# Kernel tuning notes

Hardware: AMD Instinct MI355X
Metric: run time of the kernel (lower is better)

The kernel has to match this reference:

```python
import jax, jax.numpy as jnp
import numpy as np
import math

WINDOW = 512
N_HEAD = 16

def setup_inputs() -> dict:
    key = jax.random.key(0)
    ks = jax.random.split(key, 5)
    B, L, D = 2, 4096, 1024
    s = 0.02
    return {
        "x": jax.random.normal(ks[0], (B, L, D), dtype=jnp.float32),
        "Wq": jax.random.normal(ks[1], (D, D), dtype=jnp.float32) * s,
        "bq": jnp.zeros((D,), jnp.float32),
        "Wk": jax.random.normal(ks[2], (D, D), dtype=jnp.float32) * s,
        "bk": jnp.zeros((D,), jnp.float32),
        "Wv": jax.random.normal(ks[3], (D, D), dtype=jnp.float32) * s,
        "bv": jnp.zeros((D,), jnp.float32),
        "Wo": jax.random.normal(ks[4], (D, D), dtype=jnp.float32) * s,
        "bo": jnp.zeros((D,), jnp.float32),
    }

def reference(x, Wq, bq, Wk, bk, Wv, bv, Wo, bo):
    # Chunked sliding-window MHA (eval mode, dropout inactive).
    B, L, D = x.shape
    W, H = WINDOW, N_HEAD
    dh = D // H
    C = L // W  # number of query chunks
    scale = 1.0 / math.sqrt(dh)

    # Project full sequence once (linear, per-token -> identical math).
    q = x @ Wq.T + bq
    k = x @ Wk.T + bk
    v = x @ Wv.T + bv

    # Pad K/V by one window at the front so every chunk sees 2W keys.
    kp = jnp.pad(k, ((0, 0), (W, 0), (0, 0)))
    vp = jnp.pad(v, ((0, 0), (W, 0), (0, 0)))
    idx = jnp.arange(C)[:, None] * W + jnp.arange(2 * W)[None, :]  # [C, 2W] into padded seq
    kc = kp[:, idx].reshape(B, C, 2 * W, H, dh)
    vc = vp[:, idx].reshape(B, C, 2 * W, H, dh)
    qc = q.reshape(B, C, W, H, dh)

    scores = jnp.einsum('bcqhd,bckhd->bchqk', qc, kc) * scale  # [B,C,H,W,2W]
    valid = (idx >= W)  # padded positions (chunk 0's lookback) are invalid
    scores = jnp.where(valid[None, :, None, None, :], scores, jnp.float32(-1e9))
    attn = jax.nn.softmax(scores, axis=-1)
    out = jnp.einsum('bchqk,bckhd->bcqhd', attn, vc).reshape(B, L, D)
    return out @ Wo.T + bo
```

## Files before the change

kernel.cpp:

```cpp
#include <hip/hip_runtime.h>
#include <hip/hip_bf16.h>

typedef __hip_bfloat16 bf16;
typedef __attribute__((ext_vector_type(8))) short bf16x8;
typedef __attribute__((ext_vector_type(4))) float f32x4;
typedef unsigned int u32;
typedef unsigned short u16;

#define MFMA(a,b,c) __builtin_amdgcn_mfma_f32_16x16x32_bf16((a),(b),(c),0,0,0)

__device__ __forceinline__ u16 f32_to_bf16_rtne(float f) {
  u32 b = __builtin_bit_cast(u32, f);
  b += 0x7FFFu + ((b >> 16) & 1u);
  return (u16)(b >> 16);
}
__device__ __forceinline__ u32 pk2bf(float a, float b) {
  u32 ua = __builtin_bit_cast(u32, a); ua += 0x7FFFu + ((ua >> 16) & 1u);
  u32 ub = __builtin_bit_cast(u32, b); ub += 0x7FFFu + ((ub >> 16) & 1u);
  return __builtin_amdgcn_perm(ub, ua, 0x07060302u);
}
__device__ __forceinline__ u32 pk2bf_rtz(float a, float b) {
  return __builtin_amdgcn_perm(__builtin_bit_cast(u32, b),
                               __builtin_bit_cast(u32, a), 0x07060302u);
}
__device__ __forceinline__ uint4 cvt8(uint4 lo, uint4 hi) {
  const float4 fl = __builtin_bit_cast(float4, lo);
  const float4 fh = __builtin_bit_cast(float4, hi);
  uint4 r;
  r.x = pk2bf(fl.x, fl.y); r.y = pk2bf(fl.z, fl.w);
  r.z = pk2bf(fh.x, fh.y); r.w = pk2bf(fh.z, fh.w);
  return r;
}

__device__ __forceinline__ void barrier_lgkm() {
  asm volatile("s_waitcnt lgkmcnt(0)\n\ts_barrier" ::: "memory");
}
__device__ __forceinline__ void barrier_plain() {
  asm volatile("s_barrier" ::: "memory");
}

typedef const __attribute__((address_space(1))) void* gas_ptr;
typedef __attribute__((address_space(3))) void* las_ptr;
__device__ __forceinline__ void gload_lds16(const void* g, void* l) {
  __builtin_amdgcn_global_load_lds((gas_ptr)g, (las_ptr)l, 16, 0, 0);
}

static constexpr float SL2E = 0.125f * 1.44269504f;

__global__ __launch_bounds__(256)
void cast_all(const float* __restrict__ wq, const float* __restrict__ wk,
              const float* __restrict__ wv, const float* __restrict__ wo,
              const float* __restrict__ x,
              u16* __restrict__ wqkv, u16* __restrict__ wob,
              u16* __restrict__ xb) {
  const size_t DD8 = (size_t)1024 * 1024 / 8;
  if (blockIdx.x < 2048) {
    const int m = blockIdx.x >> 9;
    const size_t i = ((size_t)(blockIdx.x & 511)) * 256 + threadIdx.x;
    const float* src = (m == 0) ? wq : (m == 1) ? wk : (m == 2) ? wv : wo;
    u16* dst = (m < 3) ? (wqkv + (size_t)m * DD8 * 8) : wob;
    const float4* s = (const float4*)src + i * 2;
    ((uint4*)dst)[i] = cvt8(__builtin_bit_cast(uint4, s[0]),
                            __builtin_bit_cast(uint4, s[1]));
  } else {
    const size_t i = ((size_t)(blockIdx.x - 2048)) * 256 + threadIdx.x;
    const float4* s = (const float4*)x + i * 2;
    ((uint4*)xb)[i] = cvt8(__builtin_bit_cast(uint4, s[0]),
                           __builtin_bit_cast(uint4, s[1]));
  }
}

template <int MODE>
__global__ __launch_bounds__(512, 2)
void gemm8p(const bf16* __restrict__ A, const bf16* __restrict__ W,
            const float* __restrict__ b0, const float* __restrict__ b1,
            const float* __restrict__ b2, void* __restrict__ o0,
            void* __restrict__ o1, void* __restrict__ o2,
            int M, int N, int K)
{
  __shared__ __align__(16) bf16 AsB[2][128 * 64];
  __shared__ __align__(16) bf16 BsB[2][256 * 64];

  const int nwg = gridDim.x * gridDim.y;
  const int raw = blockIdx.y * gridDim.x + blockIdx.x;
  const int vwg = (raw & 7) * (nwg >> 3) + (raw >> 3);
  const int NT  = gridDim.y;
  const int bx  = vwg / NT, by = vwg - bx * NT;
  const int m0  = bx * 128, n0 = by * 256;

  const int tid  = threadIdx.x;
  const int wv   = tid >> 6, lane = tid & 63;
  const int quad = lane >> 4, l16 = lane & 15;
  const int wm   = wv >> 2, wn = wv & 3;
  const int r7   = l16 & 7;

  const int rr = tid >> 3, g = tid & 7;
  const int sg8 = (g ^ (rr & 7)) * 8;
  const bf16* aS = A + (size_t)(m0 + rr) * K + sg8;
  const bf16* wS = W + (size_t)(n0 + rr) * K + sg8;
  const int ldstW = wv * 512;

#define STA8(buf, kt) do { \
    gload_lds16(aS + (size_t)(kt) * 64,                      &AsB[buf][ldstW]); \
    gload_lds16(aS + (size_t)64 * K + (size_t)(kt) * 64,     &AsB[buf][4096 + ldstW]); \
  } while (0)
#define STB8(buf, kt) do { \
    gload_lds16(wS + (size_t)(kt) * 64,                      &BsB[buf][ldstW]); \
    gload_lds16(wS + (size_t)64 * K + (size_t)(kt) * 64,     &BsB[buf][4096 + ldstW]); \
    gload_lds16(wS + (size_t)128 * K + (size_t)(kt) * 64,    &BsB[buf][8192 + ldstW]); \
    gload_lds16(wS + (size_t)192 * K + (size_t)(kt) * 64,    &BsB[buf][12288 + ldstW]); \
  } while (0)

  int aoff[4], boff[4];
#pragma unroll
  for (int mt = 0; mt < 4; ++mt) aoff[mt] = (wm * 64 + mt * 16 + l16) * 64;
#pragma unroll
  for (int nt = 0; nt < 4; ++nt) boff[nt] = (wn * 64 + nt * 16 + l16) * 64;
  const int k0o = (quad ^ r7) * 8;
  const int k1o = ((4 + quad) ^ r7) * 8;

  f32x4 acc[4][4] = {};
  bf16x8 bfr[4][2], afr[2][2];

  const int nk = K >> 6;

  STA8(0, 0);
  STB8(0, 0);
  STB8(1, 1);
  asm volatile("s_waitcnt vmcnt(4)\n\ts_barrier" ::: "memory");

  for (int t = 0; t < nk; ++t) {
    const int c = t & 1;
    const bf16* Ac = AsB[c];
    const bf16* Bc = BsB[c];

#pragma unroll
    for (int nt = 0; nt < 4; ++nt) {
      bfr[nt][0] = *(const bf16x8*)(Bc + boff[nt] + k0o);
      bfr[nt][1] = *(const bf16x8*)(Bc + boff[nt] + k1o);
    }
#pragma unroll
    for (int mt = 0; mt < 2; ++mt) {
      afr[mt][0] = *(const bf16x8*)(Ac + aoff[mt] + k0o);
      afr[mt][1] = *(const bf16x8*)(Ac + aoff[mt] + k1o);
    }
    if (t + 1 < nk) STA8((t + 1) & 1, t + 1);
    barrier_plain();
    __builtin_amdgcn_s_setprio(1);
#pragma unroll
    for (int mt = 0; mt < 2; ++mt)
#pragma unroll
      for (int nt = 0; nt < 4; ++nt) {
        acc[mt][nt] = MFMA(afr[mt][0], bfr[nt][0], acc[mt][nt]);
        acc[mt][nt] = MFMA(afr[mt][1], bfr[nt][1], acc[mt][nt]);
      }
    __builtin_amdgcn_s_setprio(0);
    barrier_lgkm();

#pragma unroll
    for (int mt = 0; mt < 2; ++mt) {
      afr[mt][0] = *(const bf16x8*)(Ac + aoff[mt + 2] + k0o);
      afr[mt][1] = *(const bf16x8*)(Ac + aoff[mt + 2] + k1o);
    }
    if (t + 2 < nk) STB8(c, t + 2);
    barrier_plain();
    __builtin_amdgcn_s_setprio(1);
#pragma unroll
    for (int mt = 0; mt < 2; ++mt)
#pragma unroll
      for (int nt = 0; nt < 4; ++nt) {
        acc[mt + 2][nt] = MFMA(afr[mt][0], bfr[nt][0], acc[mt + 2][nt]);
        acc[mt + 2][nt] = MFMA(afr[mt][1], bfr[nt][1], acc[mt + 2][nt]);
      }
    __builtin_amdgcn_s_setprio(0);
    if (t + 1 < nk) {
      if (t + 2 < nk)
        asm volatile("s_waitcnt vmcnt(4) lgkmcnt(0)\n\ts_barrier" ::: "memory");
      else
        asm volatile("s_waitcnt vmcnt(0) lgkmcnt(0)\n\ts_barrier" ::: "memory");
    }
  }
#undef STA8
#undef STB8

  const int band = n0 >> 10;
  const float* bias = (band == 0) ? b0 : (band == 1) ? b1 : b2;
#pragma unroll
  for (int nt = 0; nt < 4; ++nt) {
    const int col = n0 + wn * 64 + nt * 16 + l16;
    const int cl  = col & 1023;
    const float bv = bias[cl];
#pragma unroll
    for (int mt = 0; mt < 4; ++mt) {
      const int rbase = m0 + wm * 64 + mt * 16 + quad * 4;
      if (MODE == 1) {
#pragma unroll
        for (int r = 0; r < 4; ++r)
          ((float*)o0)[(size_t)(rbase + r) * N + col] = acc[mt][nt][r] + bv;
      } else if (band == 2) {
        const int hh = cl >> 6, dd = cl & 63;
        const int bb = rbase >> 12, tl = rbase & 4095;
        u16* dst = (u16*)o2 + ((size_t)((bb * 16 + hh) * 64 + dd)) * 4096 + tl;
        uint2 pk;
        pk.x = pk2bf(acc[mt][nt][0] + bv, acc[mt][nt][1] + bv);
        pk.y = pk2bf(acc[mt][nt][2] + bv, acc[mt][nt][3] + bv);
        *(uint2*)dst = pk;
      } else {
        u16* dst = (u16*)((band == 0) ? o0 : o1);
        const float sc = (band == 0) ? SL2E : 1.0f;
#pragma unroll
        for (int r = 0; r < 4; ++r)
          dst[(size_t)(rbase + r) * 1024 + cl] =
              f32_to_bf16_rtne((acc[mt][nt][r] + bv) * sc);
      }
    }
  }
}

__global__ __launch_bounds__(256)
void attn_swin(const bf16* __restrict__ qb, const bf16* __restrict__ kb,
               const bf16* __restrict__ vtb, u16* __restrict__ ctx)
{
  __shared__ __align__(16) bf16 Ks[2][64 * 72];
  __shared__ __align__(16) bf16 Vts[2][64 * 72];

  int bid = blockIdx.x;
  const int g  = bid & 255, qt = bid >> 8;
  const int h  = g & 15, c = (g >> 4) & 7, b = g >> 7;

  const int tid  = threadIdx.x;
  const int w    = tid >> 6, lane = tid & 63;
  const int quad = lane >> 4, l16 = lane & 15;

  const int tq0  = c * 512 + qt * 128;
  const int hoff = h * 64;
  const int kstart = (c == 0) ? 0 : (c - 1) * 512;
  const int nkt    = (c == 0) ? 8 : 16;

  bf16x8 qf[2][2];
#pragma unroll
  for (int u = 0; u < 2; ++u) {
    const bf16* qr = qb + ((size_t)(b * 4096 + tq0 + w * 32 + u * 16 + l16)) * 1024 + hoff;
    qf[u][0] = *(const bf16x8*)(qr + quad * 8);
    qf[u][1] = *(const bf16x8*)(qr + 32 + quad * 8);
  }

  const int m    = tid >> 2;
  const int cseg = (tid & 3) * 16;
  const int sig  = (((m >> 4) & 1) << 5) | (((m >> 2) & 3) << 3)
                 | (((m >> 5) & 1) << 2) | (m & 3);
  const bf16* kgp = kb + ((size_t)(b * 4096 + kstart + sig)) * 1024 + hoff + cseg;
  const bf16* vgp = vtb + ((size_t)((b * 16 + h) * 64 + m)) * 4096 + kstart + cseg;
  const int soff = m * 72 + cseg;

  float l_i[2] = {0.f, 0.f};
  f32x4 o[2][4] = {};

  uint4 ka0 = *(const uint4*)(kgp), ka1 = *(const uint4*)(kgp + 8);
  uint4 va0 = *(const uint4*)(vgp), va1 = *(const uint4*)(vgp + 8);
  kgp += (size_t)64 * 1024; vgp += 64;
  *(uint4*)(Ks[0] + soff) = ka0; *(uint4*)(Ks[0] + soff + 8) = ka1;
  *(uint4*)(Vts[0] + soff) = va0; *(uint4*)(Vts[0] + soff + 8) = va1;
  ka0 = *(const uint4*)(kgp); ka1 = *(const uint4*)(kgp + 8);
  va0 = *(const uint4*)(vgp); va1 = *(const uint4*)(vgp + 8);
  kgp += (size_t)64 * 1024; vgp += 64;
  barrier_lgkm();

  typedef union { u32 d[4]; bf16x8 v; } fragu;

  auto compute = [&](const bf16* ksb, const bf16* vtsb) {
    f32x4 s[2][4] = {};
#pragma unroll
    for (int kt = 0; kt < 4; ++kt) {
      const bf16* kr = ksb + (kt * 16 + l16) * 72;
      bf16x8 kf0 = *(const bf16x8*)(kr + quad * 8);
      bf16x8 kf1 = *(const bf16x8*)(kr + 32 + quad * 8);
      s[0][kt] = MFMA(kf0, qf[0][0], s[0][kt]);
      s[0][kt] = MFMA(kf1, qf[0][1], s[0][kt]);
      s[1][kt] = MFMA(kf0, qf[1][0], s[1][kt]);
      s[1][kt] = MFMA(kf1, qf[1][1], s[1][kt]);
    }
    fragu pf[2][2];
#pragma unroll
    for (int u = 0; u < 2; ++u) {
      float rs = 0.f;
#pragma unroll
      for (int kt = 0; kt < 4; ++kt)
#pragma unroll
        for (int r = 0; r < 4; ++r) {
          const float p = __builtin_amdgcn_exp2f(s[u][kt][r]);
          s[u][kt][r] = p;
          rs += p;
        }
      rs += __shfl_xor(rs, 16);
      rs += __shfl_xor(rs, 32);
      l_i[u] += rs;
#pragma unroll
      for (int hh = 0; hh < 2; ++hh)
#pragma unroll
        for (int dw = 0; dw < 4; ++dw) {
          const int kt = 2 * (dw >> 1) + hh, r0 = 2 * (dw & 1);
          pf[u][hh].d[dw] = pk2bf_rtz(s[u][kt][r0], s[u][kt][r0 + 1]);
        }
    }
#pragma unroll
    for (int dt = 0; dt < 4; ++dt) {
      const bf16* vr = vtsb + (dt * 16 + l16) * 72;
      bf16x8 vf0 = *(const bf16x8*)(vr + quad * 8);
      bf16x8 vf1 = *(const bf16x8*)(vr + 32 + quad * 8);
      o[0][dt] = MFMA(vf0, pf[0][0].v, o[0][dt]);
      o[0][dt] = MFMA(vf1, pf[0][1].v, o[0][dt]);
      o[1][dt] = MFMA(vf0, pf[1][0].v, o[1][dt]);
      o[1][dt] = MFMA(vf1, pf[1][1].v, o[1][dt]);
    }
  };

  for (int t = 0; t < nkt; t += 2) {
    *(uint4*)(Ks[1] + soff) = ka0; *(uint4*)(Ks[1] + soff + 8) = ka1;
    *(uint4*)(Vts[1] + soff) = va0; *(uint4*)(Vts[1] + soff + 8) = va1;
    if (t + 2 < nkt) {
      ka0 = *(const uint4*)(kgp); ka1 = *(const uint4*)(kgp + 8);
      va0 = *(const uint4*)(vgp); va1 = *(const uint4*)(vgp + 8);
      kgp += (size_t)64 * 1024; vgp += 64;
    }
    compute(Ks[0], Vts[0]);
    barrier_lgkm();

    if (t + 2 < nkt) {
      *(uint4*)(Ks[0] + soff) = ka0; *(uint4*)(Ks[0] + soff + 8) = ka1;
      *(uint4*)(Vts[0] + soff) = va0; *(uint4*)(Vts[0] + soff + 8) = va1;
      if (t + 3 < nkt) {
        ka0 = *(const uint4*)(kgp); ka1 = *(const uint4*)(kgp + 8);
        va0 = *(const uint4*)(vgp); va1 = *(const uint4*)(vgp + 8);
        kgp += (size_t)64 * 1024; vgp += 64;
      }
    }
    compute(Ks[1], Vts[1]);
    barrier_lgkm();
  }

#pragma unroll
  for (int u = 0; u < 2; ++u) {
    const float inv = 1.0f / l_i[u];
    const int qrow = tq0 + w * 32 + u * 16 + l16;
    u16* crow = ctx + ((size_t)(b * 4096 + qrow)) * 1024 + hoff;
#pragma unroll
    for (int dt = 0; dt < 4; ++dt) {
      uint2 pk;
      pk.x = pk2bf(o[u][dt][0] * inv, o[u][dt][1] * inv);
      pk.y = pk2bf(o[u][dt][2] * inv, o[u][dt][3] * inv);
      *(uint2*)(crow + dt * 16 + quad * 4) = pk;
    }
  }
}

extern "C" void kernel_launch(void* const* d_in, const int* in_sizes, int n_in,
                              void* d_out, int out_size, void* d_ws, size_t ws_size,
                              hipStream_t stream) {
  const float* x  = (const float*)d_in[0];
  const float* Wq = (const float*)d_in[1];
  const float* bq = (const float*)d_in[2];
  const float* Wk = (const float*)d_in[3];
  const float* bk = (const float*)d_in[4];
  const float* Wv = (const float*)d_in[5];
  const float* bv = (const float*)d_in[6];
  const float* Wo = (const float*)d_in[7];
  const float* bo = (const float*)d_in[8];

  const size_t MD = (size_t)8192 * 1024;
  const size_t DD = (size_t)1024 * 1024;

  char* ws = (char*)d_ws;
  u16*  Wqkvb = (u16*)ws;                     ws += 3 * DD * 2;
  u16*  Wob   = (u16*)ws;                     ws += DD * 2;
  u16*  qbuf  = (u16*)ws;                     ws += MD * 2;
  u16*  kbuf  = (u16*)ws;                     ws += MD * 2;
  u16*  vtb   = (u16*)ws;                     ws += MD * 2;
  u16*  ctx   = (u16*)ws;

  u16* xb = ctx;

  cast_all<<<dim3(6144), dim3(256), 0, stream>>>(Wq, Wk, Wv, Wo, x,
                                                 Wqkvb, Wob, xb);

  gemm8p<0><<<dim3(64, 12), dim3(512), 0, stream>>>(
      (const bf16*)xb, (const bf16*)Wqkvb, bq, bk, bv,
      qbuf, kbuf, vtb, 8192, 3072, 1024);

  attn_swin<<<dim3(1024), dim3(256), 0, stream>>>(
      (const bf16*)qbuf, (const bf16*)kbuf, (const bf16*)vtb, ctx);

  gemm8p<1><<<dim3(64, 4), dim3(512), 0, stream>>>(
      (const bf16*)ctx, (const bf16*)Wob, bo, bo, bo,
      d_out, nullptr, nullptr, 8192, 1024, 1024);
}
```

Measured before the change: 244.7 us.

## Triple-buffer GEMM LDS tiles and collapse per-iteration half-steps into one

Replaces the double-buffered, split-phase GEMM main loop (two half-iterations with interleaved A/B staging and three barriers) with a triple-buffered pipeline. Tiles for step t+2 are prefetched at the top of each iteration, and all A fragments are loaded at once, leaving one barrier per k-step. LDS usage grows to 144 KB, so launch bounds drop to one block per CU. The aim is fewer barriers and deeper prefetch, at the cost of occupancy and more fragment registers.

Result: slower. 254.1 us (+3.8%).

```diff
diff --git a/kernel.cpp b/kernel.cpp
--- a/kernel.cpp
+++ b/kernel.cpp
@@ -34,9 +34,6 @@
 
 __device__ __forceinline__ void barrier_lgkm() {
   asm volatile("s_waitcnt lgkmcnt(0)\n\ts_barrier" ::: "memory");
-}
-__device__ __forceinline__ void barrier_plain() {
-  asm volatile("s_barrier" ::: "memory");
 }
 
 typedef const __attribute__((address_space(1))) void* gas_ptr;
@@ -71,15 +68,15 @@
 }
 
 template <int MODE>
-__global__ __launch_bounds__(512, 2)
+__global__ __launch_bounds__(512, 1)
 void gemm8p(const bf16* __restrict__ A, const bf16* __restrict__ W,
             const float* __restrict__ b0, const float* __restrict__ b1,
             const float* __restrict__ b2, void* __restrict__ o0,
             void* __restrict__ o1, void* __restrict__ o2,
             int M, int N, int K)
 {
-  __shared__ __align__(16) bf16 AsB[2][128 * 64];
-  __shared__ __align__(16) bf16 BsB[2][256 * 64];
+  __shared__ __align__(16) bf16 AsB[3][128 * 64];
+  __shared__ __align__(16) bf16 BsB[3][256 * 64];
 
   const int nwg = gridDim.x * gridDim.y;
   const int raw = blockIdx.y * gridDim.x + blockIdx.x;
@@ -120,19 +117,24 @@
   const int k1o = ((4 + quad) ^ r7) * 8;
 
   f32x4 acc[4][4] = {};
-  bf16x8 bfr[4][2], afr[2][2];
+  bf16x8 bfr[4][2], afr[4][2];
 
   const int nk = K >> 6;
 
-  STA8(0, 0);
-  STB8(0, 0);
-  STB8(1, 1);
-  asm volatile("s_waitcnt vmcnt(4)\n\ts_barrier" ::: "memory");
+  STA8(0, 0); STB8(0, 0);
+  STA8(1, 1); STB8(1, 1);
+  asm volatile("s_waitcnt vmcnt(6)\n\ts_barrier" ::: "memory");
 
   for (int t = 0; t < nk; ++t) {
-    const int c = t & 1;
+    const int c = t % 3;
     const bf16* Ac = AsB[c];
     const bf16* Bc = BsB[c];
+
+    if (t + 2 < nk) {
+      const int c2 = (t + 2) % 3;
+      STA8(c2, t + 2);
+      STB8(c2, t + 2);
+    }
 
 #pragma unroll
     for (int nt = 0; nt < 4; ++nt) {
@@ -140,42 +142,24 @@
       bfr[nt][1] = *(const bf16x8*)(Bc + boff[nt] + k1o);
     }
 #pragma unroll
-    for (int mt = 0; mt < 2; ++mt) {
+    for (int mt = 0; mt < 4; ++mt) {
       afr[mt][0] = *(const bf16x8*)(Ac + aoff[mt] + k0o);
       afr[mt][1] = *(const bf16x8*)(Ac + aoff[mt] + k1o);
     }
-    if (t + 1 < nk) STA8((t + 1) & 1, t + 1);
-    barrier_plain();
+
     __builtin_amdgcn_s_setprio(1);
 #pragma unroll
-    for (int mt = 0; mt < 2; ++mt)
+    for (int mt = 0; mt < 4; ++mt)
 #pragma unroll
       for (int nt = 0; nt < 4; ++nt) {
         acc[mt][nt] = MFMA(afr[mt][0], bfr[nt][0], acc[mt][nt]);
         acc[mt][nt] = MFMA(afr[mt][1], bfr[nt][1], acc[mt][nt]);
       }
     __builtin_amdgcn_s_setprio(0);
-    barrier_lgkm();
-
-#pragma unroll
-    for (int mt = 0; mt < 2; ++mt) {
-      afr[mt][0] = *(const bf16x8*)(Ac + aoff[mt + 2] + k0o);
-      afr[mt][1] = *(const bf16x8*)(Ac + aoff[mt + 2] + k1o);
-    }
-    if (t + 2 < nk) STB8(c, t + 2);
-    barrier_plain();
-    __builtin_amdgcn_s_setprio(1);
-#pragma unroll
-    for (int mt = 0; mt < 2; ++mt)
-#pragma unroll
-      for (int nt = 0; nt < 4; ++nt) {
-        acc[mt + 2][nt] = MFMA(afr[mt][0], bfr[nt][0], acc[mt + 2][nt]);
-        acc[mt + 2][nt] = MFMA(afr[mt][1], bfr[nt][1], acc[mt + 2][nt]);
-      }
-    __builtin_amdgcn_s_setprio(0);
+
     if (t + 1 < nk) {
       if (t + 2 < nk)
-        asm volatile("s_waitcnt vmcnt(4) lgkmcnt(0)\n\ts_barrier" ::: "memory");
+        asm volatile("s_waitcnt vmcnt(6) lgkmcnt(0)\n\ts_barrier" ::: "memory");
       else
         asm volatile("s_waitcnt vmcnt(0) lgkmcnt(0)\n\ts_barrier" ::: "memory");
     }
```

## Load attention K/V fragments directly from global into registers, drop LDS staging

Applied to the files above, without the earlier changes.

The sliding-window attention kernel stops staging K and V^T tiles through shared memory with barriers. Each wave now loads its MFMA operand fragments straight from global memory into registers, prefetching the next K tile while the current one is processed. Block indices are also remapped so blocks sharing K/V land near each other for cache locality. This removes LDS traffic and block-wide syncs, but each of the four waves now fetches the same K/V data separately, which raises global/L2 traffic, and V loads are issued with little latency hiding.

Result: slower. 312.7 us (+27.8%).

```diff
diff --git a/kernel.cpp b/kernel.cpp
--- a/kernel.cpp
+++ b/kernel.cpp
@@ -30,13 +30,6 @@
   r.x = pk2bf(fl.x, fl.y); r.y = pk2bf(fl.z, fl.w);
   r.z = pk2bf(fh.x, fh.y); r.w = pk2bf(fh.z, fh.w);
   return r;
-}
-
-__device__ __forceinline__ void barrier_lgkm() {
-  asm volatile("s_waitcnt lgkmcnt(0)\n\ts_barrier" ::: "memory");
-}
-__device__ __forceinline__ void barrier_plain() {
-  asm volatile("s_barrier" ::: "memory");
 }
 
 typedef const __attribute__((address_space(1))) void* gas_ptr;
@@ -145,7 +138,7 @@
       afr[mt][1] = *(const bf16x8*)(Ac + aoff[mt] + k1o);
     }
     if (t + 1 < nk) STA8((t + 1) & 1, t + 1);
-    barrier_plain();
+    asm volatile("s_barrier" ::: "memory");
     __builtin_amdgcn_s_setprio(1);
 #pragma unroll
     for (int mt = 0; mt < 2; ++mt)
@@ -155,7 +148,7 @@
         acc[mt][nt] = MFMA(afr[mt][1], bfr[nt][1], acc[mt][nt]);
       }
     __builtin_amdgcn_s_setprio(0);
-    barrier_lgkm();
+    asm volatile("s_waitcnt lgkmcnt(0)\n\ts_barrier" ::: "memory");
 
 #pragma unroll
     for (int mt = 0; mt < 2; ++mt) {
@@ -163,7 +156,7 @@
       afr[mt][1] = *(const bf16x8*)(Ac + aoff[mt + 2] + k1o);
     }
     if (t + 2 < nk) STB8(c, t + 2);
-    barrier_plain();
+    asm volatile("s_barrier" ::: "memory");
     __builtin_amdgcn_s_setprio(1);
 #pragma unroll
     for (int mt = 0; mt < 2; ++mt)
@@ -221,12 +214,10 @@
 void attn_swin(const bf16* __restrict__ qb, const bf16* __restrict__ kb,
                const bf16* __restrict__ vtb, u16* __restrict__ ctx)
 {
-  __shared__ __align__(16) bf16 Ks[2][64 * 72];
-  __shared__ __align__(16) bf16 Vts[2][64 * 72];
-
-  int bid = blockIdx.x;
-  const int g  = bid & 255, qt = bid >> 8;
-  const int h  = g & 15, c = (g >> 4) & 7, b = g >> 7;
+  const int raw = blockIdx.x;
+  const int vb  = (raw & 7) * 128 + (raw >> 3);
+  const int qt  = vb & 3, g = vb >> 2;
+  const int h   = g & 15, c = (g >> 4) & 7, b = g >> 7;
 
   const int tid  = threadIdx.x;
   const int w    = tid >> 6, lane = tid & 63;
@@ -245,41 +236,53 @@
     qf[u][1] = *(const bf16x8*)(qr + 32 + quad * 8);
   }
 
-  const int m    = tid >> 2;
-  const int cseg = (tid & 3) * 16;
-  const int sig  = (((m >> 4) & 1) << 5) | (((m >> 2) & 3) << 3)
-                 | (((m >> 5) & 1) << 2) | (m & 3);
-  const bf16* kgp = kb + ((size_t)(b * 4096 + kstart + sig)) * 1024 + hoff + cseg;
-  const bf16* vgp = vtb + ((size_t)((b * 16 + h) * 64 + m)) * 4096 + kstart + cseg;
-  const int soff = m * 72 + cseg;
+  const int s_l = ((l16 >> 3) << 4) | (((l16 >> 2) & 1) << 3) | (l16 & 3);
+  const bf16* kR = kb + ((size_t)(b * 4096 + kstart + s_l)) * 1024 + hoff + quad * 8;
+  const bf16* vR = vtb + ((size_t)((b * 16 + h) * 64 + l16)) * 4096 + kstart + quad * 8;
+  const int ktrow[4] = {0, 32, 4, 36};
 
   float l_i[2] = {0.f, 0.f};
   f32x4 o[2][4] = {};
-
-  uint4 ka0 = *(const uint4*)(kgp), ka1 = *(const uint4*)(kgp + 8);
-  uint4 va0 = *(const uint4*)(vgp), va1 = *(const uint4*)(vgp + 8);
-  kgp += (size_t)64 * 1024; vgp += 64;
-  *(uint4*)(Ks[0] + soff) = ka0; *(uint4*)(Ks[0] + soff + 8) = ka1;
-  *(uint4*)(Vts[0] + soff) = va0; *(uint4*)(Vts[0] + soff + 8) = va1;
-  ka0 = *(const uint4*)(kgp); ka1 = *(const uint4*)(kgp + 8);
-  va0 = *(const uint4*)(vgp); va1 = *(const uint4*)(vgp + 8);
-  kgp += (size_t)64 * 1024; vgp += 64;
-  barrier_lgkm();
+  bf16x8 kf[4][2], vf[4][2];
 
   typedef union { u32 d[4]; bf16x8 v; } fragu;
 
-  auto compute = [&](const bf16* ksb, const bf16* vtsb) {
+#pragma unroll
+  for (int kt = 0; kt < 4; ++kt) {
+    const bf16* kp = kR + (size_t)ktrow[kt] * 1024;
+    kf[kt][0] = *(const bf16x8*)(kp);
+    kf[kt][1] = *(const bf16x8*)(kp + 32);
+  }
+  kR += (size_t)64 * 1024;
+
+  for (int t = 0; t < nkt; ++t) {
+#pragma unroll
+    for (int dt = 0; dt < 4; ++dt) {
+      const bf16* vp = vR + (size_t)dt * 16 * 4096;
+      vf[dt][0] = *(const bf16x8*)(vp);
+      vf[dt][1] = *(const bf16x8*)(vp + 32);
+    }
+    vR += 64;
+
     f32x4 s[2][4] = {};
 #pragma unroll
     for (int kt = 0; kt < 4; ++kt) {
-      const bf16* kr = ksb + (kt * 16 + l16) * 72;
-      bf16x8 kf0 = *(const bf16x8*)(kr + quad * 8);
-      bf16x8 kf1 = *(const bf16x8*)(kr + 32 + quad * 8);
-      s[0][kt] = MFMA(kf0, qf[0][0], s[0][kt]);
-      s[0][kt] = MFMA(kf1, qf[0][1], s[0][kt]);
-      s[1][kt] = MFMA(kf0, qf[1][0], s[1][kt]);
-      s[1][kt] = MFMA(kf1, qf[1][1], s[1][kt]);
-    }
+      s[0][kt] = MFMA(kf[kt][0], qf[0][0], s[0][kt]);
+      s[0][kt] = MFMA(kf[kt][1], qf[0][1], s[0][kt]);
+      s[1][kt] = MFMA(kf[kt][0], qf[1][0], s[1][kt]);
+      s[1][kt] = MFMA(kf[kt][1], qf[1][1], s[1][kt]);
+    }
+
+    if (t + 1 < nkt) {
+#pragma unroll
+      for (int kt = 0; kt < 4; ++kt) {
+        const bf16* kp = kR + (size_t)ktrow[kt] * 1024;
+        kf[kt][0] = *(const bf16x8*)(kp);
+        kf[kt][1] = *(const bf16x8*)(kp + 32);
+      }
+      kR += (size_t)64 * 1024;
+    }
+
     fragu pf[2][2];
 #pragma unroll
     for (int u = 0; u < 2; ++u) {
@@ -303,40 +306,14 @@
           pf[u][hh].d[dw] = pk2bf_rtz(s[u][kt][r0], s[u][kt][r0 + 1]);
         }
     }
+
 #pragma unroll
     for (int dt = 0; dt < 4; ++dt) {
-      const bf16* vr = vtsb + (dt * 16 + l16) * 72;
-      bf16x8 vf0 = *(const bf16x8*)(vr + quad * 8);
-      bf16x8 vf1 = *(const bf16x8*)(vr + 32 + quad * 8);
-      o[0][dt] = MFMA(vf0, pf[0][0].v, o[0][dt]);
-      o[0][dt] = MFMA(vf1, pf[0][1].v, o[0][dt]);
-      o[1][dt] = MFMA(vf0, pf[1][0].v, o[1][dt]);
-      o[1][dt] = MFMA(vf1, pf[1][1].v, o[1][dt]);
-    }
-  };
-
-  for (int t = 0; t < nkt; t += 2) {
-    *(uint4*)(Ks[1] + soff) = ka0; *(uint4*)(Ks[1] + soff + 8) = ka1;
-    *(uint4*)(Vts[1] + soff) = va0; *(uint4*)(Vts[1] + soff + 8) = va1;
-    if (t + 2 < nkt) {
-      ka0 = *(const uint4*)(kgp); ka1 = *(const uint4*)(kgp + 8);
-      va0 = *(const uint4*)(vgp); va1 = *(const uint4*)(vgp + 8);
-      kgp += (size_t)64 * 1024; vgp += 64;
-    }
-    compute(Ks[0], Vts[0]);
-    barrier_lgkm();
-
-    if (t + 2 < nkt) {
-      *(uint4*)(Ks[0] + soff) = ka0; *(uint4*)(Ks[0] + soff + 8) = ka1;
-      *(uint4*)(Vts[0] + soff) = va0; *(uint4*)(Vts[0] + soff + 8) = va1;
-      if (t + 3 < nkt) {
-        ka0 = *(const uint4*)(kgp); ka1 = *(const uint4*)(kgp + 8);
-        va0 = *(const uint4*)(vgp); va1 = *(const uint4*)(vgp + 8);
-        kgp += (size_t)64 * 1024; vgp += 64;
-      }
-    }
-    compute(Ks[1], Vts[1]);
-    barrier_lgkm();
+      o[0][dt] = MFMA(vf[dt][0], pf[0][0].v, o[0][dt]);
+      o[0][dt] = MFMA(vf[dt][1], pf[0][1].v, o[0][dt]);
+      o[1][dt] = MFMA(vf[dt][0], pf[1][0].v, o[1][dt]);
+      o[1][dt] = MFMA(vf[dt][1], pf[1][1].v, o[1][dt]);
+    }
   }
 
 #pragma unroll
```

## Replace output projection GEMM with smaller-tile single-buffered kernel

Applied to the files above, without the earlier changes.

The output projection no longer uses the shared 128x256 double-buffered templated GEMM. It now runs a dedicated kernel with 128x128 tiles and 256 threads, a single LDS buffer loaded by direct global-to-LDS transfers, and XOR-swizzled fragment reads. The grid grows from 256 to 512 blocks, which fills the CUs better for this N=1024 GEMM. The cost is that load latency is no longer overlapped with compute, because each K step waits at a full barrier. The QKV GEMM is de-templated, with no functional change.

Result: no change. 240.2 us (-1.9%).

```diff
diff --git a/kernel.cpp b/kernel.cpp
--- a/kernel.cpp
+++ b/kernel.cpp
@@ -34,9 +34,6 @@
 
 __device__ __forceinline__ void barrier_lgkm() {
   asm volatile("s_waitcnt lgkmcnt(0)\n\ts_barrier" ::: "memory");
-}
-__device__ __forceinline__ void barrier_plain() {
-  asm volatile("s_barrier" ::: "memory");
 }
 
 typedef const __attribute__((address_space(1))) void* gas_ptr;
@@ -70,13 +67,12 @@
   }
 }
 
-template <int MODE>
 __global__ __launch_bounds__(512, 2)
-void gemm8p(const bf16* __restrict__ A, const bf16* __restrict__ W,
-            const float* __restrict__ b0, const float* __restrict__ b1,
-            const float* __restrict__ b2, void* __restrict__ o0,
-            void* __restrict__ o1, void* __restrict__ o2,
-            int M, int N, int K)
+void gemm_qkv(const bf16* __restrict__ A, const bf16* __restrict__ W,
+              const float* __restrict__ b0, const float* __restrict__ b1,
+              const float* __restrict__ b2, u16* __restrict__ o0,
+              u16* __restrict__ o1, u16* __restrict__ o2,
+              int M, int N, int K)
 {
   __shared__ __align__(16) bf16 AsB[2][128 * 64];
   __shared__ __align__(16) bf16 BsB[2][256 * 64];
@@ -145,7 +141,7 @@
       afr[mt][1] = *(const bf16x8*)(Ac + aoff[mt] + k1o);
     }
     if (t + 1 < nk) STA8((t + 1) & 1, t + 1);
-    barrier_plain();
+    asm volatile("s_barrier" ::: "memory");
     __builtin_amdgcn_s_setprio(1);
 #pragma unroll
     for (int mt = 0; mt < 2; ++mt)
@@ -155,7 +151,7 @@
         acc[mt][nt] = MFMA(afr[mt][1], bfr[nt][1], acc[mt][nt]);
       }
     __builtin_amdgcn_s_setprio(0);
-    barrier_lgkm();
+    asm volatile("s_waitcnt lgkmcnt(0)\n\ts_barrier" ::: "memory");
 
 #pragma unroll
     for (int mt = 0; mt < 2; ++mt) {
@@ -163,7 +159,7 @@
       afr[mt][1] = *(const bf16x8*)(Ac + aoff[mt + 2] + k1o);
     }
     if (t + 2 < nk) STB8(c, t + 2);
-    barrier_plain();
+    asm volatile("s_barrier" ::: "memory");
     __builtin_amdgcn_s_setprio(1);
 #pragma unroll
     for (int mt = 0; mt < 2; ++mt)
@@ -193,26 +189,98 @@
 #pragma unroll
     for (int mt = 0; mt < 4; ++mt) {
       const int rbase = m0 + wm * 64 + mt * 16 + quad * 4;
-      if (MODE == 1) {
-#pragma unroll
-        for (int r = 0; r < 4; ++r)
-          ((float*)o0)[(size_t)(rbase + r) * N + col] = acc[mt][nt][r] + bv;
-      } else if (band == 2) {
+      if (band == 2) {
         const int hh = cl >> 6, dd = cl & 63;
         const int bb = rbase >> 12, tl = rbase & 4095;
-        u16* dst = (u16*)o2 + ((size_t)((bb * 16 + hh) * 64 + dd)) * 4096 + tl;
+        u16* dst = o2 + ((size_t)((bb * 16 + hh) * 64 + dd)) * 4096 + tl;
         uint2 pk;
         pk.x = pk2bf(acc[mt][nt][0] + bv, acc[mt][nt][1] + bv);
         pk.y = pk2bf(acc[mt][nt][2] + bv, acc[mt][nt][3] + bv);
         *(uint2*)dst = pk;
       } else {
-        u16* dst = (u16*)((band == 0) ? o0 : o1);
+        u16* dst = (band == 0) ? o0 : o1;
         const float sc = (band == 0) ? SL2E : 1.0f;
 #pragma unroll
         for (int r = 0; r < 4; ++r)
           dst[(size_t)(rbase + r) * 1024 + cl] =
               f32_to_bf16_rtne((acc[mt][nt][r] + bv) * sc);
       }
+    }
+  }
+}
+
+__global__ __launch_bounds__(256)
+void gemm_out(const bf16* __restrict__ A, const bf16* __restrict__ W,
+              const float* __restrict__ bias, float* __restrict__ out,
+              int M, int N, int K)
+{
+  __shared__ bf16 As[128 * 64];
+  __shared__ bf16 Bs[128 * 64];
+
+  const int tid  = threadIdx.x;
+  const int wave = tid >> 6, lane = tid & 63;
+  const int quad = lane >> 4, l16 = lane & 15;
+  const int wm   = wave >> 1, wn  = wave & 1;
+  const int m0   = blockIdx.x * 128, n0 = blockIdx.y * 128;
+
+  const int srow = lane >> 3;
+  const int sg   = lane & 7;
+  const size_t rgs = (size_t)8 * K;
+  const bf16* aSrc = A + (size_t)(m0 + wave * 32 + srow) * K + ((sg ^ srow) * 8);
+  const bf16* wSrc = W + (size_t)(n0 + wave * 32 + srow) * K + ((sg ^ srow) * 8);
+  bf16* aB = As + wave * 32 * 64;
+  bf16* wB = Bs + wave * 32 * 64;
+
+  const int niter = K >> 6;
+
+  f32x4 acc[4][4] = {};
+
+  const int arow[4] = { (wm * 64 + 0 * 16 + l16) * 64, (wm * 64 + 1 * 16 + l16) * 64,
+                        (wm * 64 + 2 * 16 + l16) * 64, (wm * 64 + 3 * 16 + l16) * 64 };
+  const int brow[4] = { (wn * 64 + 0 * 16 + l16) * 64, (wn * 64 + 1 * 16 + l16) * 64,
+                        (wn * 64 + 2 * 16 + l16) * 64, (wn * 64 + 3 * 16 + l16) * 64 };
+  const int r7 = l16 & 7;
+
+  for (int t = 0; t < niter; ++t) {
+    gload_lds16(aSrc,            aB);
+    gload_lds16(aSrc + rgs,      aB + 512);
+    gload_lds16(aSrc + 2 * rgs,  aB + 1024);
+    gload_lds16(aSrc + 3 * rgs,  aB + 1536);
+    gload_lds16(wSrc,            wB);
+    gload_lds16(wSrc + rgs,      wB + 512);
+    gload_lds16(wSrc + 2 * rgs,  wB + 1024);
+    gload_lds16(wSrc + 3 * rgs,  wB + 1536);
+    aSrc += 64; wSrc += 64;
+    __syncthreads();
+
+#pragma unroll
+    for (int kk = 0; kk < 2; ++kk) {
+      bf16x8 af[4], bw[4];
+#pragma unroll
+      for (int mt = 0; mt < 4; ++mt)
+        af[mt] = *(const bf16x8*)(As + arow[mt] + (((kk * 4 + quad) ^ r7) * 8));
+#pragma unroll
+      for (int nt = 0; nt < 4; ++nt)
+        bw[nt] = *(const bf16x8*)(Bs + brow[nt] + (((kk * 4 + quad) ^ r7) * 8));
+#pragma unroll
+      for (int mt = 0; mt < 4; ++mt)
+#pragma unroll
+        for (int nt = 0; nt < 4; ++nt)
+          acc[mt][nt] = MFMA(af[mt], bw[nt], acc[mt][nt]);
+    }
+    if (t + 1 < niter) __syncthreads();
+  }
+
+#pragma unroll
+  for (int nt = 0; nt < 4; ++nt) {
+    const int col = n0 + wn * 64 + nt * 16 + l16;
+    const float bv = bias[col & 1023];
+#pragma unroll
+    for (int mt = 0; mt < 4; ++mt) {
+      const int rbase = m0 + wm * 64 + mt * 16 + quad * 4;
+#pragma unroll
+      for (int r = 0; r < 4; ++r)
+        out[(size_t)(rbase + r) * N + col] = acc[mt][nt][r] + bv;
     }
   }
 }
@@ -383,14 +451,13 @@
   cast_all<<<dim3(6144), dim3(256), 0, stream>>>(Wq, Wk, Wv, Wo, x,
                                                  Wqkvb, Wob, xb);
 
-  gemm8p<0><<<dim3(64, 12), dim3(512), 0, stream>>>(
+  gemm_qkv<<<dim3(64, 12), dim3(512), 0, stream>>>(
       (const bf16*)xb, (const bf16*)Wqkvb, bq, bk, bv,
       qbuf, kbuf, vtb, 8192, 3072, 1024);
 
   attn_swin<<<dim3(1024), dim3(256), 0, stream>>>(
       (const bf16*)qbuf, (const bf16*)kbuf, (const bf16*)vtb, ctx);
 
-  gemm8p<1><<<dim3(64, 4), dim3(512), 0, stream>>>(
-      (const bf16*)ctx, (const bf16*)Wob, bo, bo, bo,
-      d_out, nullptr, nullptr, 8192, 1024, 1024);
-}
+  gemm_out<<<dim3(64, 8), dim3(256), 0, stream>>>(
+      (const bf16*)ctx, (const bf16*)Wob, bo, (float*)d_out, 8192, 1024, 1024);
+}
```
